# Kernel optimization log

Measured on AMD Instinct MI355X. Metric: run time of the kernel, lower is better.

## Reference

```python
import jax, jax.numpy as jnp
import numpy as np
from math import factorial as fact

L_MAX = 3
K = 128
N = 8192

# ---- Clebsch-Gordan coefficients (Racah formula, real for integer l) ----

def _cg_coeff(l1, m1, l2, m2, l3, m3):
    if m1 + m2 != m3:
        return 0.0
    pref = ((2 * l3 + 1) * fact(l3 + l1 - l2) * fact(l3 - l1 + l2)
            * fact(l1 + l2 - l3) / fact(l1 + l2 + l3 + 1)) ** 0.5
    pref *= (fact(l3 + m3) * fact(l3 - m3) * fact(l1 - m1) * fact(l1 + m1)
             * fact(l2 - m2) * fact(l2 + m2)) ** 0.5
    s = 0.0
    for k in range(max(0, l2 - l3 - m1, l1 - l3 + m2),
                   min(l1 + l2 - l3, l1 - m1, l2 + m2) + 1):
        s += (-1) ** k / (fact(k) * fact(l1 + l2 - l3 - k) * fact(l1 - m1 - k)
                          * fact(l2 + m2 - k) * fact(l3 - l2 + m1 + k)
                          * fact(l3 - l1 - m2 + k))
    return pref * s


def _cg_tensor(l1, l2, l3):
    C = np.zeros((2 * l1 + 1, 2 * l2 + 1, 2 * l3 + 1), dtype=np.float32)
    for m1 in range(-l1, l1 + 1):
        for m2 in range(-l2, l2 + 1):
            m3 = m1 + m2
            if -l3 <= m3 <= l3:
                C[m1 + l1, m2 + l2, m3 + l3] = _cg_coeff(l1, m1, l2, m2, l3, m3)
    return jnp.asarray(C)

# all allowed (l1, l2, l3) coupling paths, deterministic order
PATHS = [(l1, l2, l3)
         for l1 in range(L_MAX + 1)
         for l2 in range(L_MAX + 1)
         for l3 in range(abs(l1 - l2), min(l1 + l2, L_MAX) + 1)]
CG = {p: _cg_tensor(*p) for p in PATHS}
N_PATHS = [sum(1 for p in PATHS if p[2] == l3) for l3 in range(L_MAX + 1)]  # [4,9,11,10]


def setup_inputs() -> dict:
    key = jax.random.key(0)
    ks = jax.random.split(key, 12)
    inp = {}
    for i, l in enumerate(range(L_MAX + 1)):
        inp[f"f1_l{l}"] = jax.random.normal(ks[i], (N, 2 * l + 1, K), jnp.float32)
        inp[f"f2_l{l}"] = jax.random.normal(ks[4 + i], (N, 2 * l + 1, K), jnp.float32)
        fan_in = N_PATHS[l] * K
        inp[f"W_l{l}"] = jax.random.normal(ks[8 + i], (fan_in, K), jnp.float32) / np.sqrt(fan_in)
    return inp


def _forward(f1, f2, W):
    # CG tensor product: per-path contraction, channel-wise in k
    tp = [[] for _ in range(L_MAX + 1)]
    for (l1, l2, l3) in PATHS:
        C = CG[(l1, l2, l3)]  # [2l1+1, 2l2+1, 2l3+1]
        tp[l3].append(jnp.einsum('abm,nak,nbk->nmk', C, f1[l1], f2[l2]))
    # concat paths along channels, linear mix back to K, residual add
    outs = []
    for l3 in range(L_MAX + 1):
        cat = jnp.concatenate(tp[l3], axis=-1)        # [N, 2l3+1, n_paths*K]
        mixed = jnp.einsum('nmp,pk->nmk', cat, W[l3])  # [N, 2l3+1, K]
        outs.append(f1[l3] + mixed)
    return tuple(outs)


def reference(f1_l0, f1_l1, f1_l2, f1_l3,
              f2_l0, f2_l1, f2_l2, f2_l3,
              W_l0, W_l1, W_l2, W_l3):
    f1 = [f1_l0, f1_l1, f1_l2, f1_l3]
    f2 = [f2_l0, f2_l1, f2_l2, f2_l3]
    W = [W_l0, W_l1, W_l2, W_l3]
    return _forward(f1, f2, W)
```

## Files before the change

kernel.cpp:

```cpp
#include <hip/hip_runtime.h>

#define K_DIM 128

typedef __attribute__((ext_vector_type(8))) short short8;
typedef __attribute__((ext_vector_type(4))) float f32x4;
typedef __attribute__((ext_vector_type(2))) float f32x2;

constexpr int C_L1[34] = {0,0,0,0, 1,1,1,1,1,1,1,1,1, 2,2,2,2,2,2,2,2,2,2,2, 3,3,3,3,3,3,3,3,3,3};
constexpr int C_L2[34] = {0,1,2,3, 0,1,1,1,2,2,2,3,3, 0,1,1,1,2,2,2,2,3,3,3, 0,1,1,2,2,2,3,3,3,3};
constexpr int C_L3[34] = {0,1,2,3, 1,0,1,2,1,2,3,2,3, 2,1,2,3,0,1,2,3,1,2,3, 3,2,3,1,2,3,0,1,2,3};
constexpr int C_NP[4]  = {4,9,11,10};
constexpr int C_PL[4][11] = {
  {0,5,17,30, 0,0,0,0,0,0,0},
  {1,4,6,8,14,18,21,27,31, 0,0},
  {2,7,9,11,13,15,19,22,25,28,32},
  {3,10,12,16,20,23,24,26,29,33, 0}
};
constexpr int C_CSUM[4] = {0,8,26,48};
constexpr size_t FOFF[4] = {0, 1048576, 4194304, 9437184};
constexpr int FSZ[4] = {1048576, 3145728, 5242880, 7340032};
constexpr size_t FTOT = 16777216;

__device__ double dfactd(int n){ double r=1.0; for(int i=2;i<=n;++i) r*=(double)i; return r; }

__device__ __forceinline__ unsigned short f2bf(float x) {
    unsigned int b = __float_as_uint(x);
    return (unsigned short)((b + 0x7FFFu + ((b >> 16) & 1u)) >> 16);
}
__device__ __forceinline__ float bflo(unsigned int u){ return __uint_as_float(u << 16); }
__device__ __forceinline__ float bfhi(unsigned int u){ return __uint_as_float(u & 0xFFFF0000u); }

__device__ __forceinline__ unsigned int cvtpk(float lo, float hi) {
    unsigned int r;
    asm("v_cvt_pk_bf16_f32 %0, %1, %2" : "=v"(r) : "v"(lo), "v"(hi));
    return r;
}
__device__ __forceinline__ f32x2 pk_mul(f32x2 a, f32x2 b) {
    f32x2 d;
    asm("v_pk_mul_f32 %0, %1, %2" : "=v"(d) : "v"(a), "v"(b));
    return d;
}
__device__ __forceinline__ f32x2 pk_fma(f32x2 a, f32x2 b, f32x2 c) {
    f32x2 d;
    asm("v_pk_fma_f32 %0, %1, %2, %3" : "=v"(d) : "v"(a), "v"(b), "v"(c));
    return d;
}

__global__ void cg_init(float* __restrict__ C2) {
    int e = blockIdx.x*blockDim.x + threadIdx.x;
    if (e >= 34*49) return;
    int p = e/49, r = e%49, m1i = r/7, m2i = r%7;
    int l1 = C_L1[p], l2 = C_L2[p], l3 = C_L3[p];
    float val = 0.f;
    if (m1i < 2*l1+1 && m2i < 2*l2+1) {
        int m1 = m1i-l1, m2 = m2i-l2, m3 = m1+m2;
        if (m3 >= -l3 && m3 <= l3) {
            double pref = sqrt((double)(2*l3+1) * dfactd(l3+l1-l2)*dfactd(l3-l1+l2)
                               * dfactd(l1+l2-l3) / dfactd(l1+l2+l3+1));
            pref *= sqrt(dfactd(l3+m3)*dfactd(l3-m3)*dfactd(l1-m1)*dfactd(l1+m1)
                         *dfactd(l2-m2)*dfactd(l2+m2));
            int kmin = max(0, max(l2-l3-m1, l1-l3+m2));
            int kmax = min(l1+l2-l3, min(l1-m1, l2+m2));
            double s = 0.0;
            for (int k=kmin;k<=kmax;++k) {
                double t = dfactd(k)*dfactd(l1+l2-l3-k)*dfactd(l1-m1-k)
                         * dfactd(l2+m2-k)*dfactd(l3-l2+m1+k)*dfactd(l3-l1-m2+k);
                s += ((k&1)? -1.0:1.0)/t;
            }
            val = (float)(pref*s);
        }
    }
    C2[e] = val;
}

__global__ void wt_prep(const float* __restrict__ W0, const float* __restrict__ W1,
                        const float* __restrict__ W2, const float* __restrict__ W3,
                        unsigned short* __restrict__ wt) {
    int b = blockIdx.x;
    int chunk = b >> 5;
    int e = ((b & 31) << 8) + threadIdx.x;
    int kk = e & 63, col = e >> 6;
    int l3 = (chunk < 8) ? 0 : (chunk < 26) ? 1 : (chunk < 48) ? 2 : 3;
    int local = chunk - C_CSUM[l3];
    int kin = local*64 + kk;
    const float* W = (l3==0)?W0:(l3==1)?W1:(l3==2)?W2:W3;
    float v = W[(size_t)kin*K_DIM + col];
    wt[(size_t)chunk*8192 + col*64 + (kk ^ ((col&7)<<3))] = f2bf(v);
}

__global__ void fpack(const float* __restrict__ s0, const float* __restrict__ s1,
                      const float* __restrict__ s2, const float* __restrict__ s3,
                      const float* __restrict__ s4, const float* __restrict__ s5,
                      const float* __restrict__ s6, const float* __restrict__ s7,
                      unsigned short* __restrict__ dst) {
    int y = blockIdx.y;
    int l = y & 3, fi = y >> 2;
    const float* srcs[8] = {s0,s1,s2,s3,s4,s5,s6,s7};
    const float* src = srcs[y];
    int i4 = blockIdx.x*256 + threadIdx.x;
    if (i4*4 >= FSZ[l]) return;
    float4 v = reinterpret_cast<const float4*>(src)[i4];
    unsigned int u0 = (unsigned int)f2bf(v.x) | ((unsigned int)f2bf(v.y) << 16);
    unsigned int u1 = (unsigned int)f2bf(v.z) | ((unsigned int)f2bf(v.w) << 16);
    unsigned short* d = dst + fi*FTOT + FOFF[l] + (size_t)i4*4;
    *reinterpret_cast<uint2*>(d) = make_uint2(u0, u1);
}

template<int L3, int PI>
__device__ __forceinline__ void tp_into(
    const unsigned int (&q1)[16][2], const unsigned int (&q2s)[7][2],
    const f32x2* __restrict__ C2slot, unsigned char* __restrict__ Ab,
    int nodel, int chq)
{
    constexpr int P  = C_PL[L3][PI];
    constexpr int l1 = C_L1[P], l2 = C_L2[P];
    constexpr int d1 = 2*l1+1, d2 = 2*l2+1;
    constexpr int TL3 = 2*L3+1;
    #pragma unroll
    for (int h=0; h<2; ++h) {
        f32x2 x[d1];
        #pragma unroll
        for (int m=0;m<d1;++m) x[m] = (f32x2){bflo(q1[l1*l1+m][h]), bfhi(q1[l1*l1+m][h])};
        f32x2 a[TL3];
        #pragma unroll
        for (int mt=0;mt<TL3;++mt) a[mt] = (f32x2){0.f, 0.f};
        #pragma unroll
        for (int m2i=0; m2i<d2; ++m2i) {
            f32x2 y = (f32x2){bflo(q2s[m2i][h]), bfhi(q2s[m2i][h])};
            #pragma unroll
            for (int m1i=0; m1i<d1; ++m1i) {
                int mt = (m1i-l1) + (m2i-l2) + L3;
                if (mt >= 0 && mt < TL3) {
                    f32x2 c2 = C2slot[m1i*7 + m2i];
                    a[mt] = pk_fma(pk_mul(x[m1i], y), c2, a[mt]);
                }
            }
        }
        #pragma unroll
        for (int mt=0; mt<TL3; ++mt) {
            int row = nodel*TL3 + mt;
            *reinterpret_cast<unsigned int*>(
                Ab + row*256 + h*128 + ((chq*4) ^ ((row&7)<<4))) = cvtpk(a[mt][0], a[mt][1]);
        }
    }
}

template<int L3, int PI>
__device__ __forceinline__ void stream_f2(
    const unsigned short* __restrict__ f2b, int n0, int nodel, int chq,
    unsigned int (&q2s)[7][2])
{
    constexpr int P  = C_PL[L3][PI];
    constexpr int l2 = C_L2[P];
    constexpr int d2 = 2*l2+1;
    const unsigned short* g2 = f2b + FOFF[l2] + (size_t)(n0+nodel)*(d2*128) + chq*2;
    #pragma unroll
    for (int m=0;m<d2;++m) {
        q2s[m][0] = *reinterpret_cast<const unsigned int*>(g2 + m*128);
        q2s[m][1] = *reinterpret_cast<const unsigned int*>(g2 + m*128 + 64);
    }
}

template<int L3, int PI>
__device__ __forceinline__ void load_wf(const unsigned short* __restrict__ wt,
                                        int col, int lg, short8 (&wf)[4]) {
    const int wkey = (col&7)<<4;
    const unsigned char* wb0 = (const unsigned char*)(wt + (size_t)(C_CSUM[L3] + PI*2    )*8192);
    const unsigned char* wb1 = (const unsigned char*)(wt + (size_t)(C_CSUM[L3] + PI*2 + 1)*8192);
    wf[0] = *reinterpret_cast<const short8*>(wb0 + col*128 + ((16*lg     ) ^ wkey));
    wf[1] = *reinterpret_cast<const short8*>(wb0 + col*128 + ((16*lg + 64) ^ wkey));
    wf[2] = *reinterpret_cast<const short8*>(wb1 + col*128 + ((16*lg     ) ^ wkey));
    wf[3] = *reinterpret_cast<const short8*>(wb1 + col*128 + ((16*lg + 64) ^ wkey));
}

template<int L3>
__device__ __forceinline__ void mfma_from(
    const unsigned char* __restrict__ Ab, const short8 (&wf)[4],
    int lr, int lg, f32x4 (&cacc)[2*L3+1])
{
    constexpr int TL3 = 2*L3+1;
    #pragma unroll
    for (int kst=0; kst<4; ++kst) {
        #pragma unroll
        for (int rt=0; rt<TL3; ++rt) {
            int arow = 16*rt + lr;
            short8 af = *reinterpret_cast<const short8*>(
                Ab + arow*256 + ((16*lg + 64*kst) ^ ((arow&7)<<4)));
            cacc[rt] = __builtin_amdgcn_mfma_f32_16x16x32_bf16(af, wf[kst], cacc[rt], 0, 0, 0);
        }
    }
}

template<int L3, int PI>
__device__ __forceinline__ void pipe(
    const unsigned int (&q1)[16][2], unsigned int (&q2s)[7][2],
    const unsigned short* __restrict__ f2b,
    const unsigned short* __restrict__ wt, const float* __restrict__ C2,
    f32x2 (&C2s)[2][49], unsigned char* A0, unsigned char* A1,
    int tid, int n0, int nodel, int chq, int col, int lr, int lg,
    f32x4 (&cacc)[2*L3+1])
{
    constexpr int NP = C_NP[L3];
    short8 wf[4];
    load_wf<L3, PI>(wt, col, lg, wf);
    if constexpr (PI+2 < NP) {
        if (tid < 49) {
            float v = C2[C_PL[L3][PI+2]*49 + tid];
            C2s[PI&1][tid] = (f32x2){v, v};
        }
    }
    if constexpr (PI+1 < NP) {
        stream_f2<L3, PI+1>(f2b, n0, nodel, chq, q2s);
        tp_into<L3, PI+1>(q1, q2s, C2s[(PI+1)&1], ((PI+1)&1) ? A1 : A0, nodel, chq);
    }
    mfma_from<L3>((PI&1) ? A1 : A0, wf, lr, lg, cacc);
    __syncthreads();
    if constexpr (PI+1 < NP)
        pipe<L3, PI+1>(q1, q2s, f2b, wt, C2, C2s, A0, A1,
                       tid, n0, nodel, chq, col, lr, lg, cacc);
}

template<int L3>
__device__ __forceinline__ void run16(
    int n0,
    const unsigned short* __restrict__ f1b, const unsigned short* __restrict__ f2b,
    const unsigned short* __restrict__ wt, const float* __restrict__ C2,
    float* __restrict__ out, f32x2 (&C2s)[2][49], unsigned char* Asb)
{
    constexpr int TL3 = 2*L3+1;
    constexpr int NP  = C_NP[L3];
    const int tid   = threadIdx.x;
    const int nodel = tid >> 5;
    const int chq   = tid & 31;
    const int lane  = tid & 63, wid = tid >> 6;
    const int lr    = lane & 15, lg = lane >> 4;
    const int col   = 16*wid + lr;
    constexpr size_t OB = FOFF[L3];
    unsigned char* A0 = Asb;
    unsigned char* A1 = Asb + 28672;

    unsigned int q1[16][2];
    #pragma unroll
    for (int l=0; l<4; ++l) {
        const unsigned short* g1 = f1b + FOFF[l] + (size_t)(n0+nodel)*((2*l+1)*128) + chq*2;
        #pragma unroll
        for (int m=0; m<2*l+1; ++m) {
            q1[l*l+m][0] = *reinterpret_cast<const unsigned int*>(g1 + m*128);
            q1[l*l+m][1] = *reinterpret_cast<const unsigned int*>(g1 + m*128 + 64);
        }
    }
    unsigned int q2s[7][2];

    f32x4 cacc[TL3];
    #pragma unroll
    for (int rt=0; rt<TL3; ++rt) cacc[rt] = (f32x4){0.f,0.f,0.f,0.f};

    if (tid < 49) {
        float v0 = C2[C_PL[L3][0]*49 + tid];
        C2s[0][tid] = (f32x2){v0, v0};
        if constexpr (NP > 1) {
            float v1 = C2[C_PL[L3][1]*49 + tid];
            C2s[1][tid] = (f32x2){v1, v1};
        }
    }
    __syncthreads();
    stream_f2<L3, 0>(f2b, n0, nodel, chq, q2s);
    tp_into<L3, 0>(q1, q2s, C2s[0], A0, nodel, chq);
    __syncthreads();
    pipe<L3, 0>(q1, q2s, f2b, wt, C2, C2s, A0, A1,
                tid, n0, nodel, chq, col, lr, lg, cacc);

    float* S = reinterpret_cast<float*>(Asb);
    const unsigned short* __restrict__ fr = f1b + OB;
    #pragma unroll
    for (int rt0=0; rt0<TL3; rt0+=4) {
        const int bn = (TL3 - rt0 < 4) ? (TL3 - rt0) : 4;
        #pragma unroll
        for (int rtl=0; rtl<4; ++rtl) {
            if (rtl < bn) {
                #pragma unroll
                for (int i=0;i<4;++i)
                    S[(rtl*16 + 4*lg + i)*132 + col] = cacc[rt0+rtl][i];
            }
        }
        __syncthreads();
        #pragma unroll
        for (int it=0; it<4; ++it) {
            if (it < bn) {
                int s = tid + it*512;
                int rows = s >> 5, cq = (s & 31) * 4;
                int gr = n0*TL3 + (rt0 + (rows >> 4))*16 + (rows & 15);
                size_t ro = (size_t)gr * K_DIM;
                float4 v = *reinterpret_cast<const float4*>(&S[rows*132 + cq]);
                uint2 rb = *reinterpret_cast<const uint2*>(fr + ro + cq);
                v.x += bflo(rb.x); v.y += bfhi(rb.x);
                v.z += bflo(rb.y); v.w += bfhi(rb.y);
                *reinterpret_cast<float4*>(&out[OB + ro + cq]) = v;
            }
        }
        __syncthreads();
    }
}

__global__ __launch_bounds__(512) void cg_main(
    const unsigned short* __restrict__ f1b, const unsigned short* __restrict__ f2b,
    const unsigned short* __restrict__ wt,
    const float* __restrict__ C2, float* __restrict__ out)
{
    __shared__ __align__(16) unsigned char Asb[2*28672];
    __shared__ f32x2 C2s[2][49];

    int bid = blockIdx.x;
    int x = bid & 7, j = bid >> 3;
    int rnd = j >> 4, k = j & 15;
    int l3 = k >> 2, q = k & 3;
    int n0 = x*1024 + rnd*64 + q*16;
    if (l3 == 0)      run16<0>(n0, f1b, f2b, wt, C2, out, C2s, Asb);
    else if (l3 == 1) run16<1>(n0, f1b, f2b, wt, C2, out, C2s, Asb);
    else if (l3 == 2) run16<2>(n0, f1b, f2b, wt, C2, out, C2s, Asb);
    else              run16<3>(n0, f1b, f2b, wt, C2, out, C2s, Asb);
}

extern "C" void kernel_launch(void* const* d_in, const int* in_sizes, int n_in,
                              void* d_out, int out_size, void* d_ws, size_t ws_size,
                              hipStream_t stream) {
    const float* f10 = (const float*)d_in[0];
    const float* f20 = (const float*)d_in[1];
    const float* W0  = (const float*)d_in[2];
    const float* f11 = (const float*)d_in[3];
    const float* f21 = (const float*)d_in[4];
    const float* W1  = (const float*)d_in[5];
    const float* f12 = (const float*)d_in[6];
    const float* f22 = (const float*)d_in[7];
    const float* W2  = (const float*)d_in[8];
    const float* f13 = (const float*)d_in[9];
    const float* f23 = (const float*)d_in[10];
    const float* W3  = (const float*)d_in[11];

    float* C2 = (float*)d_ws;
    unsigned short* wtw = (unsigned short*)((char*)d_ws + 8192);
    unsigned short* f1b = (unsigned short*)((char*)d_ws + 1122304);
    unsigned short* f2b = f1b + FTOT;
    float* out = (float*)d_out;

    hipLaunchKernelGGL(cg_init, dim3(7), dim3(256), 0, stream, C2);
    hipLaunchKernelGGL(wt_prep, dim3(68*32), dim3(256), 0, stream, W0, W1, W2, W3, wtw);
    hipLaunchKernelGGL(fpack, dim3(7168, 8), dim3(256), 0, stream,
        f10, f11, f12, f13, f20, f21, f22, f23, f1b);
    hipLaunchKernelGGL(cg_main, dim3(2048), dim3(512), 0, stream,
        f1b, f2b, wtw, C2, out);
}
```

Before: 162.9 us.

## Preload all CG coefficients to LDS and reorder pipeline to overlap f2 loads with MFMA

Loads every path's CG coefficient block into shared memory once at kernel start instead of double-buffering two paths at a time. In each pipeline stage, the next path's f2 global loads are issued before the MFMA phase and the tensor-product build is moved after it, so load latency is hidden behind matrix math. MFMA sections are also wrapped in s_setprio to raise wave priority during matrix work. This costs extra LDS for the coefficient table and keeps the f2 registers live across the MFMA block, which may raise register pressure.

```diff
diff --git a/kernel.cpp b/kernel.cpp
--- a/kernel.cpp
+++ b/kernel.cpp
@@ -11,6 +11,12 @@
 constexpr int C_L3[34] = {0,1,2,3, 1,0,1,2,1,2,3,2,3, 2,1,2,3,0,1,2,3,1,2,3, 3,2,3,1,2,3,0,1,2,3};
 constexpr int C_NP[4]  = {4,9,11,10};
 constexpr int C_PL[4][11] = {
+  {0,5,17,30, 0,0,0,0,0,0,0},
+  {1,4,6,8,14,18,21,27,31, 0,0},
+  {2,7,9,11,13,15,19,22,25,28,32},
+  {3,10,12,16,20,23,24,26,29,33, 0}
+};
+__device__ const int D_PL[4][11] = {
   {0,5,17,30, 0,0,0,0,0,0,0},
   {1,4,6,8,14,18,21,27,31, 0,0},
   {2,7,9,11,13,15,19,22,25,28,32},
@@ -179,6 +185,7 @@
     int lr, int lg, f32x4 (&cacc)[2*L3+1])
 {
     constexpr int TL3 = 2*L3+1;
+    __builtin_amdgcn_s_setprio(1);
     #pragma unroll
     for (int kst=0; kst<4; ++kst) {
         #pragma unroll
@@ -189,34 +196,29 @@
             cacc[rt] = __builtin_amdgcn_mfma_f32_16x16x32_bf16(af, wf[kst], cacc[rt], 0, 0, 0);
         }
     }
+    __builtin_amdgcn_s_setprio(0);
 }
 
 template<int L3, int PI>
 __device__ __forceinline__ void pipe(
     const unsigned int (&q1)[16][2], unsigned int (&q2s)[7][2],
     const unsigned short* __restrict__ f2b,
-    const unsigned short* __restrict__ wt, const float* __restrict__ C2,
-    f32x2 (&C2s)[2][49], unsigned char* A0, unsigned char* A1,
+    const unsigned short* __restrict__ wt,
+    const f32x2 (&C2all)[11][49], unsigned char* A0, unsigned char* A1,
     int tid, int n0, int nodel, int chq, int col, int lr, int lg,
     f32x4 (&cacc)[2*L3+1])
 {
     constexpr int NP = C_NP[L3];
+    if constexpr (PI+1 < NP)
+        stream_f2<L3, PI+1>(f2b, n0, nodel, chq, q2s);
     short8 wf[4];
     load_wf<L3, PI>(wt, col, lg, wf);
-    if constexpr (PI+2 < NP) {
-        if (tid < 49) {
-            float v = C2[C_PL[L3][PI+2]*49 + tid];
-            C2s[PI&1][tid] = (f32x2){v, v};
-        }
-    }
-    if constexpr (PI+1 < NP) {
-        stream_f2<L3, PI+1>(f2b, n0, nodel, chq, q2s);
-        tp_into<L3, PI+1>(q1, q2s, C2s[(PI+1)&1], ((PI+1)&1) ? A1 : A0, nodel, chq);
-    }
     mfma_from<L3>((PI&1) ? A1 : A0, wf, lr, lg, cacc);
+    if constexpr (PI+1 < NP)
+        tp_into<L3, PI+1>(q1, q2s, C2all[PI+1], ((PI+1)&1) ? A1 : A0, nodel, chq);
     __syncthreads();
     if constexpr (PI+1 < NP)
-        pipe<L3, PI+1>(q1, q2s, f2b, wt, C2, C2s, A0, A1,
+        pipe<L3, PI+1>(q1, q2s, f2b, wt, C2all, A0, A1,
                        tid, n0, nodel, chq, col, lr, lg, cacc);
 }
 
@@ -225,7 +227,7 @@
     int n0,
     const unsigned short* __restrict__ f1b, const unsigned short* __restrict__ f2b,
     const unsigned short* __restrict__ wt, const float* __restrict__ C2,
-    float* __restrict__ out, f32x2 (&C2s)[2][49], unsigned char* Asb)
+    float* __restrict__ out, f32x2 (&C2all)[11][49], unsigned char* Asb)
 {
     constexpr int TL3 = 2*L3+1;
     constexpr int NP  = C_NP[L3];
@@ -239,6 +241,12 @@
     unsigned char* A0 = Asb;
     unsigned char* A1 = Asb + 28672;
 
+    for (int i = tid; i < NP*49; i += 512) {
+        int pi = i / 49, r = i - pi*49;
+        float v = C2[D_PL[L3][pi]*49 + r];
+        C2all[pi][r] = (f32x2){v, v};
+    }
+
     unsigned int q1[16][2];
     #pragma unroll
     for (int l=0; l<4; ++l) {
@@ -255,19 +263,11 @@
     #pragma unroll
     for (int rt=0; rt<TL3; ++rt) cacc[rt] = (f32x4){0.f,0.f,0.f,0.f};
 
-    if (tid < 49) {
-        float v0 = C2[C_PL[L3][0]*49 + tid];
-        C2s[0][tid] = (f32x2){v0, v0};
-        if constexpr (NP > 1) {
-            float v1 = C2[C_PL[L3][1]*49 + tid];
-            C2s[1][tid] = (f32x2){v1, v1};
-        }
-    }
     __syncthreads();
     stream_f2<L3, 0>(f2b, n0, nodel, chq, q2s);
-    tp_into<L3, 0>(q1, q2s, C2s[0], A0, nodel, chq);
+    tp_into<L3, 0>(q1, q2s, C2all[0], A0, nodel, chq);
     __syncthreads();
-    pipe<L3, 0>(q1, q2s, f2b, wt, C2, C2s, A0, A1,
+    pipe<L3, 0>(q1, q2s, f2b, wt, C2all, A0, A1,
                 tid, n0, nodel, chq, col, lr, lg, cacc);
 
     float* S = reinterpret_cast<float*>(Asb);
@@ -308,17 +308,17 @@
     const float* __restrict__ C2, float* __restrict__ out)
 {
     __shared__ __align__(16) unsigned char Asb[2*28672];
-    __shared__ f32x2 C2s[2][49];
+    __shared__ f32x2 C2all[11][49];
 
     int bid = blockIdx.x;
     int x = bid & 7, j = bid >> 3;
     int rnd = j >> 4, k = j & 15;
     int l3 = k >> 2, q = k & 3;
     int n0 = x*1024 + rnd*64 + q*16;
-    if (l3 == 0)      run16<0>(n0, f1b, f2b, wt, C2, out, C2s, Asb);
-    else if (l3 == 1) run16<1>(n0, f1b, f2b, wt, C2, out, C2s, Asb);
-    else if (l3 == 2) run16<2>(n0, f1b, f2b, wt, C2, out, C2s, Asb);
-    else              run16<3>(n0, f1b, f2b, wt, C2, out, C2s, Asb);
+    if (l3 == 0)      run16<0>(n0, f1b, f2b, wt, C2, out, C2all, Asb);
+    else if (l3 == 1) run16<1>(n0, f1b, f2b, wt, C2, out, C2all, Asb);
+    else if (l3 == 2) run16<2>(n0, f1b, f2b, wt, C2, out, C2all, Asb);
+    else              run16<3>(n0, f1b, f2b, wt, C2, out, C2all, Asb);
 }
 
 extern "C" void kernel_launch(void* const* d_in, const int* in_sizes, int n_in,
```

Result: no change. 161.5 us (-0.9%).
